# Performance work log

Hardware: AMD Instinct MI355X
Metric: run time of the kernel (lower is better)

The kernel has to match this reference:

```python
import jax, jax.numpy as jnp
import numpy as np

B, H, S, D = 2, 12, 1024, 128
KQ, KK = 6, 11  # per-head conv kernel over (query, key) score plane


def setup_inputs() -> dict:
    key = jax.random.key(0)
    kq, kk, kv, kw = jax.random.split(key, 4)
    Q = jax.random.normal(kq, (B, H, S, D), dtype=jnp.float32)
    K = jax.random.normal(kk, (B, H, S, D), dtype=jnp.float32)
    V = jax.random.normal(kv, (B, H, S, D), dtype=jnp.float32)
    W = jax.random.normal(kw, (H, KQ, KK), dtype=jnp.float32) * 0.1
    return {"Q": Q, "K": K, "V": V, "W": W}


def reference(Q, K, V, W):
    # causal=True, softmax_scale = 1/sqrt(head_dim)  (module defaults)
    b, h, s, d = Q.shape
    _, kq, kk = W.shape
    pad_q = kq - 1            # causal padding along the query axis
    pad_k = (kk - 1) // 2     # 'same' padding along the key axis
    scale = 1.0 / np.sqrt(d).astype(np.float32)

    # Raw QK^T scores: [b, h, s_q, s_k]
    scores = jnp.einsum('bhqd,bhkd->bhqk', Q, K)

    # Causal: zero out future keys before the conv so the kernel cannot mix
    # in future information (matches the `causal` flag passed into the
    # fused qk_conv kernel; out-of-range tiles load as 0 in the Triton code).
    tril = jnp.tril(jnp.ones((s, s), dtype=bool))
    scores = jnp.where(tril[None, None], scores, 0.0)

    # Per-head 2D conv over the (q, k) plane: grouped conv with H groups,
    # kernel W[h] applied to head h's score map. Cross-correlation (PyTorch
    # conv semantics == lax.conv_general_dilated without kernel flip).
    conv = jax.lax.conv_general_dilated(
        scores,                      # [b, h, s, s] as NCHW
        W[:, None, :, :],            # [h, 1, kq, kk] as OIHW, groups=h
        window_strides=(1, 1),
        padding=((pad_q, 0), (pad_k, pad_k)),
        feature_group_count=h,
        dimension_numbers=('NCHW', 'OIHW', 'NCHW'),
    )

    # Scale, re-apply causal mask with the kernel's -1e6 fill, softmax, @V.
    logits = conv * scale + jnp.where(tril[None, None], 0.0, -1000000.0)
    P = jax.nn.softmax(logits, axis=-1)
    O = jnp.einsum('bhqk,bhkd->bhqd', P, V)
    return O
```

## Files before the change

### kernel.cpp

```cpp
#include <hip/hip_runtime.h>
#include <hip/hip_bf16.h>
#include <math.h>

#define B_ 2
#define H_ 12
#define S_ 1024
#define D_ 128
#define BH_ (B_ * H_)
#define SCALE 0.08838834764831843f

#define QPAD 16
#define QROWS (S_ + QPAD)

#define NB_KH   768
#define NB_QP   3120
#define NB_VT   3072
#define NB_PREPA (NB_KH + NB_QP + NB_VT)

typedef __attribute__((ext_vector_type(8))) short short8;
typedef __attribute__((ext_vector_type(4))) float floatx4;

__device__ __forceinline__ unsigned short f2b(float f) {
    return __builtin_bit_cast(unsigned short, __float2bfloat16(f));
}

__global__ __launch_bounds__(256) void prep_a_kernel(
    const float* __restrict__ Q, const float* __restrict__ K,
    const float* __restrict__ V, const float* __restrict__ W,
    unsigned short* __restrict__ Qp, unsigned short* __restrict__ KhF,
    unsigned short* __restrict__ VhF)
{
    __shared__ __align__(16) union {
        float kld[42][132];
        float vt_ls[32][33];
    } sm;
    const int blk = blockIdx.x;
    const int tid = threadIdx.x;

    if (blk < NB_KH) {
        const int bh = blk >> 5, kt = blk & 31;
        const int h = bh % H_;
        const int k0 = kt * 32;
        for (int p = tid; p < 42 * 32; p += 256) {
            const int r = p >> 5, c4 = (p & 31) * 4;
            const int gk = k0 - 5 + r;
            float4 v = make_float4(0.f, 0.f, 0.f, 0.f);
            if (gk >= 0 && gk < S_)
                v = *(const float4*)(K + ((size_t)bh * S_ + gk) * D_ + c4);
            *(float4*)&sm.kld[r][c4] = v;
        }
        __syncthreads();
        const int wv = tid >> 6, ln = tid & 63;
        const float* Wh = W + h * 66;
        const size_t obase = (size_t)blk * 24576;
        #pragma unroll
        for (int nt = 0; nt < 2; ++nt) {
            const int lr = nt * 16 + (ln & 15);
            const int d0 = wv * 32 + (ln >> 4) * 8;
            float a[6][8];
            #pragma unroll
            for (int i = 0; i < 6; ++i)
                #pragma unroll
                for (int e = 0; e < 8; ++e) a[i][e] = 0.f;
            #pragma unroll
            for (int j = 0; j < 11; ++j) {
                const float4 v0 = *(const float4*)&sm.kld[lr + j][d0];
                const float4 v1 = *(const float4*)&sm.kld[lr + j][d0 + 4];
                #pragma unroll
                for (int i = 0; i < 6; ++i) {
                    const float w = Wh[i * 11 + j];
                    a[i][0] += w * v0.x; a[i][1] += w * v0.y;
                    a[i][2] += w * v0.z; a[i][3] += w * v0.w;
                    a[i][4] += w * v1.x; a[i][5] += w * v1.y;
                    a[i][6] += w * v1.z; a[i][7] += w * v1.w;
                }
            }
            #pragma unroll
            for (int i = 0; i < 6; ++i) {
                short8 o;
                #pragma unroll
                for (int e = 0; e < 8; ++e) o[e] = (short)f2b(a[i][e] * SCALE);
                *(short8*)(KhF + obase + (size_t)(((i * 4 + wv) * 2 + nt) * 64 + ln) * 8) = o;
            }
        }
    } else if (blk < NB_KH + NB_QP) {
        const int idx = (blk - NB_KH) * 256 + tid;
        const size_t e0 = (size_t)idx * 4;
        const int bh = (int)(e0 / ((size_t)QROWS * D_));
        const int rem = (int)(e0 - (size_t)bh * QROWS * D_);
        const int r = rem / D_;
        const int d = rem - r * D_;
        const int sr = r - QPAD;
        float4 v = make_float4(0.f, 0.f, 0.f, 0.f);
        if (sr >= 0 && sr < S_)
            v = *(const float4*)(Q + ((size_t)bh * S_ + sr) * D_ + d);
        ushort4 o; o.x = f2b(v.x); o.y = f2b(v.y); o.z = f2b(v.z); o.w = f2b(v.w);
        *(ushort4*)(Qp + ((size_t)bh * QROWS + r) * D_ + d) = o;
    } else {
        const int b2 = blk - (NB_KH + NB_QP);
        const int dt = b2 & 3, ktl = (b2 >> 2) & 31, bh = b2 >> 7;
        const int lk = tid >> 3, ld = (tid & 7) * 4;
        const float4 v4 = *(const float4*)(V + ((size_t)bh * S_ + ktl * 32 + lk) * D_ + dt * 32 + ld);
        sm.vt_ls[lk][ld + 0] = v4.x; sm.vt_ls[lk][ld + 1] = v4.y;
        sm.vt_ls[lk][ld + 2] = v4.z; sm.vt_ls[lk][ld + 3] = v4.w;
        __syncthreads();
        const int lk2 = tid >> 3, lc = (tid & 7) * 4;
        const int pb = ((lc >> 3) << 2) | (((lc >> 2) & 1) << 4);
        const int d = dt * 32 + lk2;
        const int nd = d >> 4, l15v = d & 15;
        ushort4 o;
        o.x = f2b(sm.vt_ls[pb + 0][lk2]); o.y = f2b(sm.vt_ls[pb + 1][lk2]);
        o.z = f2b(sm.vt_ls[pb + 2][lk2]); o.w = f2b(sm.vt_ls[pb + 3][lk2]);
        const size_t addr = ((size_t)((bh * 32 + ktl) * 8 + nd) * 64
                             + (lc >> 3) * 16 + l15v) * 8 + (lc & 7);
        *(ushort4*)(VhF + addr) = o;
    }
}

__global__ __launch_bounds__(256) void prep_corr_kernel(
    const float* __restrict__ Q, const float* __restrict__ K,
    const float* __restrict__ W, float* __restrict__ Corr)
{
    __shared__ __align__(16) struct {
        float Ks[78][132];
        float band[69][16];
    } sm;
    const int cb = blockIdx.x;
    const int tid = threadIdx.x;
    const int bh = cb >> 4, q0c = (cb & 15) * 64;
    const int h = bh % H_;

    for (int p = tid; p < 78 * 32; p += 256) {
        const int r = p >> 5, c4 = (p & 31) * 4;
        const int gk = q0c - 4 + r;
        float4 v = make_float4(0.f, 0.f, 0.f, 0.f);
        if (gk >= 0 && gk < S_)
            v = *(const float4*)(K + ((size_t)bh * S_ + gk) * D_ + c4);
        *(float4*)&sm.Ks[r][c4] = v;
    }
    __syncthreads();
    for (int s = tid; s < 69 * 16; s += 256) {
        const int r = s >> 4, dsl = s & 15;
        float v = 0.f;
        const int qp = q0c - 5 + r;
        if (dsl < 10 && qp >= 0 && qp + dsl + 1 < S_) {
            const float4* qr = (const float4*)(Q + ((size_t)bh * S_ + qp) * D_);
            const float4* kr = (const float4*)&sm.Ks[r + dsl][0];
            #pragma unroll 8
            for (int c = 0; c < 32; ++c) {
                const float4 a = qr[c], b = kr[c];
                v += a.x * b.x + a.y * b.y + a.z * b.z + a.w * b.w;
            }
        }
        sm.band[r][dsl] = v;
    }
    __syncthreads();
    for (int e = tid; e < 64 * 16; e += 256) {
        const int ql = e >> 4, d = e & 15;
        float v = 0.f;
        if (d <= 10) {
            for (int i2 = 0; i2 < 6; ++i2)
                for (int j = i2 + d + 1; j < 11; ++j)
                    v += W[h * 66 + i2 * 11 + j] * SCALE * sm.band[ql + i2][j - i2 - d - 1];
        }
        Corr[((size_t)bh << 14) + ((size_t)(q0c + ql) << 4) + d] = v;
    }
}

__global__ __launch_bounds__(256, 3) void conv_attn_mfma(
    const unsigned short* __restrict__ Qp,
    const unsigned short* __restrict__ KhF,
    const unsigned short* __restrict__ VhF,
    const float* __restrict__ Corr,
    float* __restrict__ O,
    float* __restrict__ Op1, float* __restrict__ Op2, float* __restrict__ Op3,
    float* __restrict__ L0, float* __restrict__ L1,
    float* __restrict__ L2, float* __restrict__ L3)
{
    const int tid = threadIdx.x;
    const int wv = tid >> 6;
    const int ln = tid & 63;
    const int l15 = ln & 15;
    const int qd = ln >> 4;

    const int bid = blockIdx.x;
    const int xcd = bid & 7;
    const int slot = bid >> 3;
    const int bh = xcd * 3 + slot / 64;
    const int inner = slot & 63;
    const int sg = 15 - (inner >> 2);
    const int ks = inner & 3;

    const int s = sg * 4 + wv;
    const int qw0 = s * 16;
    const int ktw = s >> 1;
    const int n = ktw + 1;
    const int qtr = n >> 2, rem = n & 3;
    const int cnt = qtr + (ks < rem ? 1 : 0);
    const int klo = ks * qtr + (ks < rem ? ks : rem);

    const unsigned short* Khb = KhF + (size_t)(bh * 32) * 24576 + ln * 8;
    const unsigned short* Vhb = VhF + (size_t)(bh * 32) * 4096 + ln * 8;
    const float* Cb = Corr + ((size_t)bh << 14);

    short8 qf[6][4];
    {
        const unsigned short* qbase =
            Qp + ((size_t)bh * QROWS + qw0 + 11 + l15) * D_ + qd * 8;
        #pragma unroll
        for (int i = 0; i < 6; ++i)
            #pragma unroll
            for (int kc = 0; kc < 4; ++kc)
                qf[i][kc] = *(const short8*)(qbase + (size_t)i * D_ + kc * 32);
    }

    floatx4 acc[8];
    #pragma unroll
    for (int nd = 0; nd < 8; ++nd) acc[nd] = (floatx4){0.f, 0.f, 0.f, 0.f};
    float l_run = 0.f;

    for (int t = 0; t < cnt; ++t) {
        const int kt = klo + t;
        const int k0 = kt * 32;
        const unsigned short* A = Khb + (size_t)kt * 24576;

        short8 vf[8];
        #pragma unroll
        for (int nd = 0; nd < 8; ++nd)
            vf[nd] = *(const short8*)(Vhb + (size_t)kt * 4096 + nd * 512);

        floatx4 s0 = {0.f, 0.f, 0.f, 0.f}, s1 = {0.f, 0.f, 0.f, 0.f};
        #pragma unroll
        for (int c = 0; c < 24; ++c) {
            const short8 a0 = *(const short8*)(A + c * 1024);
            const short8 a1 = *(const short8*)(A + c * 1024 + 512);
            const short8 b = qf[c >> 2][c & 3];
            s0 = __builtin_amdgcn_mfma_f32_16x16x32_bf16(a0, b, s0, 0, 0, 0);
            s1 = __builtin_amdgcn_mfma_f32_16x16x32_bf16(a1, b, s1, 0, 0, 0);
        }

        const bool need_corr = (kt >= ktw - 1);
        const int qrow = qw0 + l15;
        float sum = 0.f;
        short8 pbv;
        #pragma unroll
        for (int nt = 0; nt < 2; ++nt)
            #pragma unroll
            for (int rg = 0; rg < 4; ++rg) {
                const int kcol = k0 + nt * 16 + qd * 4 + rg;
                float v = nt ? s1[rg] : s0[rg];
                if (need_corr) {
                    const int dd = qrow - kcol;
                    if (dd >= 0 && dd <= 10) v -= Cb[(qrow << 4) + dd];
                }
                const float p = (kcol <= qrow) ? __expf(v) : 0.f;
                sum += p;
                pbv[nt * 4 + rg] = (short)f2b(p);
            }
        sum += __shfl_xor(sum, 16);
        sum += __shfl_xor(sum, 32);
        l_run += sum;

        #pragma unroll
        for (int nd = 0; nd < 8; ++nd)
            acc[nd] = __builtin_amdgcn_mfma_f32_16x16x32_bf16(pbv, vf[nd], acc[nd], 0, 0, 0);
    }

    float* Ob = (ks == 0) ? O : (ks == 1) ? Op1 : (ks == 2) ? Op2 : Op3;
    float* Lb = (ks == 0) ? L0 : (ks == 1) ? L1 : (ks == 2) ? L2 : L3;
    if (qd == 0) Lb[bh * S_ + qw0 + l15] = l_run;
    #pragma unroll
    for (int rg = 0; rg < 4; ++rg) {
        const int row = qw0 + qd * 4 + rg;
        float* orow = Ob + ((size_t)bh * S_ + row) * D_;
        #pragma unroll
        for (int nd = 0; nd < 8; ++nd)
            orow[nd * 16 + l15] = acc[nd][rg];
    }
}

__global__ __launch_bounds__(256) void merge_kernel(
    float* __restrict__ O,
    const float* __restrict__ Op1, const float* __restrict__ Op2,
    const float* __restrict__ Op3,
    const float* __restrict__ L0, const float* __restrict__ L1,
    const float* __restrict__ L2, const float* __restrict__ L3)
{
    const int idx = blockIdx.x * 256 + threadIdx.x;
    const int row = idx >> 5;
    const float inv = 1.f / (L0[row] + L1[row] + L2[row] + L3[row]);
    const float4 a = ((const float4*)O)[idx];
    const float4 b = ((const float4*)Op1)[idx];
    const float4 c = ((const float4*)Op2)[idx];
    const float4 d = ((const float4*)Op3)[idx];
    float4 o;
    o.x = (a.x + b.x + c.x + d.x) * inv;
    o.y = (a.y + b.y + c.y + d.y) * inv;
    o.z = (a.z + b.z + c.z + d.z) * inv;
    o.w = (a.w + b.w + c.w + d.w) * inv;
    ((float4*)O)[idx] = o;
}

extern "C" void kernel_launch(void* const* d_in, const int* in_sizes, int n_in,
                              void* d_out, int out_size, void* d_ws, size_t ws_size,
                              hipStream_t stream) {
    const float* Q = (const float*)d_in[0];
    const float* K = (const float*)d_in[1];
    const float* V = (const float*)d_in[2];
    const float* W = (const float*)d_in[3];
    float* O = (float*)d_out;

    unsigned short* Qp  = (unsigned short*)d_ws;
    unsigned short* KhF = (unsigned short*)((char*)d_ws + 6389760);
    unsigned short* VhF = (unsigned short*)((char*)d_ws + 44138496);
    float*          Cr  = (float*)((char*)d_ws + 50429952);
    float*          Op1 = (float*)((char*)d_ws + 52002816);
    float*          Op2 = (float*)((char*)d_ws + 64585728);
    float*          Op3 = (float*)((char*)d_ws + 77168640);
    float*          L0  = (float*)((char*)d_ws + 89751552);
    float*          L1  = (float*)((char*)d_ws + 89849856);
    float*          L2  = (float*)((char*)d_ws + 89948160);
    float*          L3  = (float*)((char*)d_ws + 90046464);

    prep_a_kernel<<<dim3(NB_PREPA), dim3(256), 0, stream>>>(Q, K, V, W, Qp, KhF, VhF);
    prep_corr_kernel<<<dim3(384), dim3(256), 0, stream>>>(Q, K, W, Cr);
    conv_attn_mfma<<<dim3(1536), dim3(256), 0, stream>>>(Qp, KhF, VhF, Cr, O,
                                                         Op1, Op2, Op3, L0, L1, L2, L3);
    merge_kernel<<<dim3(3072), dim3(256), 0, stream>>>(O, Op1, Op2, Op3, L0, L1, L2, L3);
}
```

Baseline: 249.8 us.

## Process 32 query rows per block with LDS-staged Q and split-K across waves

Each block now handles a 32-row query tile. The four waves split the key tiles among themselves instead of each wave owning a 16-row query strip. Q fragments (37 rows, padded stride) are staged once into shared memory and read per MFMA, rather than held in 24 registers per wave. Each K/V fragment loaded from global memory now feeds two query sub-tiles, which doubles reuse of K and V loads and halves the block count. In exchange there are LDS reads in the inner loop, twice as many accumulators, and a changed load balance and grid size.

```diff
diff --git a/kernel.cpp b/kernel.cpp
--- a/kernel.cpp
+++ b/kernel.cpp
@@ -177,47 +177,43 @@
     float* __restrict__ L0, float* __restrict__ L1,
     float* __restrict__ L2, float* __restrict__ L3)
 {
+    __shared__ __align__(16) unsigned short qs[37 * 136];
+
     const int tid = threadIdx.x;
-    const int wv = tid >> 6;
+    const int ks = tid >> 6;
     const int ln = tid & 63;
     const int l15 = ln & 15;
     const int qd = ln >> 4;
 
     const int bid = blockIdx.x;
-    const int xcd = bid & 7;
     const int slot = bid >> 3;
-    const int bh = xcd * 3 + slot / 64;
-    const int inner = slot & 63;
-    const int sg = 15 - (inner >> 2);
-    const int ks = inner & 3;
-
-    const int s = sg * 4 + wv;
-    const int qw0 = s * 16;
-    const int ktw = s >> 1;
-    const int n = ktw + 1;
-    const int qtr = n >> 2, rem = n & 3;
-    const int cnt = qtr + (ks < rem ? 1 : 0);
-    const int klo = ks * qtr + (ks < rem ? ks : rem);
+    const int bh = (bid & 7) * 3 + slot / 32;
+    const int qb = slot & 31;
+
+    for (int p = tid; p < 37 * 16; p += 256) {
+        const int r = p >> 4, c = p & 15;
+        *(short8*)&qs[r * 136 + c * 8] =
+            *(const short8*)(Qp + ((size_t)bh * QROWS + qb * 32 + 11 + r) * D_ + c * 8);
+    }
+    __syncthreads();
+
+    const int ktw = qb;
+    const int n = qb + 1;
+    const int base = n >> 2, rem = n & 3;
+    const int cnt = base + (ks < rem ? 1 : 0);
+    const int klo = ks * base + (ks < rem ? ks : rem);
 
     const unsigned short* Khb = KhF + (size_t)(bh * 32) * 24576 + ln * 8;
     const unsigned short* Vhb = VhF + (size_t)(bh * 32) * 4096 + ln * 8;
     const float* Cb = Corr + ((size_t)bh << 14);
 
-    short8 qf[6][4];
-    {
-        const unsigned short* qbase =
-            Qp + ((size_t)bh * QROWS + qw0 + 11 + l15) * D_ + qd * 8;
-        #pragma unroll
-        for (int i = 0; i < 6; ++i)
-            #pragma unroll
-            for (int kc = 0; kc < 4; ++kc)
-                qf[i][kc] = *(const short8*)(qbase + (size_t)i * D_ + kc * 32);
-    }
-
-    floatx4 acc[8];
+    floatx4 acc[2][8];
     #pragma unroll
-    for (int nd = 0; nd < 8; ++nd) acc[nd] = (floatx4){0.f, 0.f, 0.f, 0.f};
-    float l_run = 0.f;
+    for (int mt = 0; mt < 2; ++mt)
+        #pragma unroll
+        for (int nd = 0; nd < 8; ++nd)
+            acc[mt][nd] = (floatx4){0.f, 0.f, 0.f, 0.f};
+    float l_run[2] = {0.f, 0.f};
 
     for (int t = 0; t < cnt; ++t) {
         const int kt = klo + t;
@@ -229,54 +225,77 @@
         for (int nd = 0; nd < 8; ++nd)
             vf[nd] = *(const short8*)(Vhb + (size_t)kt * 4096 + nd * 512);
 
-        floatx4 s0 = {0.f, 0.f, 0.f, 0.f}, s1 = {0.f, 0.f, 0.f, 0.f};
+        floatx4 sc_[2][2];
+        #pragma unroll
+        for (int nt = 0; nt < 2; ++nt)
+            #pragma unroll
+            for (int mt = 0; mt < 2; ++mt)
+                sc_[nt][mt] = (floatx4){0.f, 0.f, 0.f, 0.f};
+
         #pragma unroll
         for (int c = 0; c < 24; ++c) {
             const short8 a0 = *(const short8*)(A + c * 1024);
             const short8 a1 = *(const short8*)(A + c * 1024 + 512);
-            const short8 b = qf[c >> 2][c & 3];
-            s0 = __builtin_amdgcn_mfma_f32_16x16x32_bf16(a0, b, s0, 0, 0, 0);
-            s1 = __builtin_amdgcn_mfma_f32_16x16x32_bf16(a1, b, s1, 0, 0, 0);
+            const int r0 = l15 + (c >> 2);
+            const int co = (c & 3) * 32 + qd * 8;
+            const short8 b0 = *(const short8*)&qs[r0 * 136 + co];
+            const short8 b1 = *(const short8*)&qs[(r0 + 16) * 136 + co];
+            sc_[0][0] = __builtin_amdgcn_mfma_f32_16x16x32_bf16(a0, b0, sc_[0][0], 0, 0, 0);
+            sc_[0][1] = __builtin_amdgcn_mfma_f32_16x16x32_bf16(a0, b1, sc_[0][1], 0, 0, 0);
+            sc_[1][0] = __builtin_amdgcn_mfma_f32_16x16x32_bf16(a1, b0, sc_[1][0], 0, 0, 0);
+            sc_[1][1] = __builtin_amdgcn_mfma_f32_16x16x32_bf16(a1, b1, sc_[1][1], 0, 0, 0);
         }
 
         const bool need_corr = (kt >= ktw - 1);
-        const int qrow = qw0 + l15;
-        float sum = 0.f;
-        short8 pbv;
-        #pragma unroll
-        for (int nt = 0; nt < 2; ++nt)
-            #pragma unroll
-            for (int rg = 0; rg < 4; ++rg) {
-                const int kcol = k0 + nt * 16 + qd * 4 + rg;
-                float v = nt ? s1[rg] : s0[rg];
-                if (need_corr) {
-                    const int dd = qrow - kcol;
-                    if (dd >= 0 && dd <= 10) v -= Cb[(qrow << 4) + dd];
+        short8 pfrag[2];
+        #pragma unroll
+        for (int mt = 0; mt < 2; ++mt) {
+            const int qrow = qb * 32 + mt * 16 + l15;
+            float sum = 0.f;
+            short8 pbv;
+            #pragma unroll
+            for (int nt = 0; nt < 2; ++nt)
+                #pragma unroll
+                for (int rg = 0; rg < 4; ++rg) {
+                    const int kcol = k0 + nt * 16 + qd * 4 + rg;
+                    float v = sc_[nt][mt][rg];
+                    if (need_corr) {
+                        const int dd = qrow - kcol;
+                        if (dd >= 0 && dd <= 10) v -= Cb[(qrow << 4) + dd];
+                    }
+                    const float p = (kcol <= qrow) ? __expf(v) : 0.f;
+                    sum += p;
+                    pbv[nt * 4 + rg] = (short)f2b(p);
                 }
-                const float p = (kcol <= qrow) ? __expf(v) : 0.f;
-                sum += p;
-                pbv[nt * 4 + rg] = (short)f2b(p);
-            }
-        sum += __shfl_xor(sum, 16);
-        sum += __shfl_xor(sum, 32);
-        l_run += sum;
+            sum += __shfl_xor(sum, 16);
+            sum += __shfl_xor(sum, 32);
+            l_run[mt] += sum;
+            pfrag[mt] = pbv;
+        }
 
         #pragma unroll
         for (int nd = 0; nd < 8; ++nd)
-            acc[nd] = __builtin_amdgcn_mfma_f32_16x16x32_bf16(pbv, vf[nd], acc[nd], 0, 0, 0);
+            #pragma unroll
+            for (int mt = 0; mt < 2; ++mt)
+                acc[mt][nd] = __builtin_amdgcn_mfma_f32_16x16x32_bf16(pfrag[mt], vf[nd], acc[mt][nd], 0, 0, 0);
     }
 
     float* Ob = (ks == 0) ? O : (ks == 1) ? Op1 : (ks == 2) ? Op2 : Op3;
     float* Lb = (ks == 0) ? L0 : (ks == 1) ? L1 : (ks == 2) ? L2 : L3;
-    if (qd == 0) Lb[bh * S_ + qw0 + l15] = l_run;
+    if (qd == 0) {
+        Lb[bh * S_ + qb * 32 + l15] = l_run[0];
+        Lb[bh * S_ + qb * 32 + 16 + l15] = l_run[1];
+    }
     #pragma unroll
-    for (int rg = 0; rg < 4; ++rg) {
-        const int row = qw0 + qd * 4 + rg;
-        float* orow = Ob + ((size_t)bh * S_ + row) * D_;
-        #pragma unroll
-        for (int nd = 0; nd < 8; ++nd)
-            orow[nd * 16 + l15] = acc[nd][rg];
-    }
+    for (int mt = 0; mt < 2; ++mt)
+        #pragma unroll
+        for (int rg = 0; rg < 4; ++rg) {
+            const int row = qb * 32 + mt * 16 + qd * 4 + rg;
+            float* orow = Ob + ((size_t)bh * S_ + row) * D_;
+            #pragma unroll
+            for (int nd = 0; nd < 8; ++nd)
+                orow[nd * 16 + l15] = acc[mt][nd][rg];
+        }
 }
 
 __global__ __launch_bounds__(256) void merge_kernel(
@@ -324,7 +343,7 @@
 
     prep_a_kernel<<<dim3(NB_PREPA), dim3(256), 0, stream>>>(Q, K, V, W, Qp, KhF, VhF);
     prep_corr_kernel<<<dim3(384), dim3(256), 0, stream>>>(Q, K, W, Cr);
-    conv_attn_mfma<<<dim3(1536), dim3(256), 0, stream>>>(Qp, KhF, VhF, Cr, O,
-                                                         Op1, Op2, Op3, L0, L1, L2, L3);
+    conv_attn_mfma<<<dim3(768), dim3(256), 0, stream>>>(Qp, KhF, VhF, Cr, O,
+                                                        Op1, Op2, Op3, L0, L1, L2, L3);
     merge_kernel<<<dim3(3072), dim3(256), 0, stream>>>(O, Op1, Op2, Op3, L0, L1, L2, L3);
 }
```

Measured after the change: 323.9 us. 29.6% more time.
